# Kernel tuning notes

Hardware: AMD Instinct MI355X
Metric: run time of the kernel (lower is better)

The kernel has to match this reference:

```python
import jax, jax.numpy as jnp
import numpy as np

# ---- dimensions ----
N = 16384      # nodes
E = 131072     # edges (avg degree 8)
F = 128        # scalar channel width == s_dim
L = 9          # spherical-harmonic components (lmax=2)
R = 8          # radial basis size
DOUT = L * F   # post-product node width (1152)
K = 1024       # fixed number of master nodes (static stand-in for m>0.5)
HID = 64       # master-selection hidden dim
DA = 64        # virtual-attention head dim
LAMBDA_ATTN = 0.5
R_CUT = 5.0
EPS = 1e-9


def sh_l2(u):
    # real SH polynomials up to l=2 on unit vectors u[..., 3] -> [..., 9]
    x, y, z = u[..., 0], u[..., 1], u[..., 2]
    o = jnp.ones_like(x)
    return jnp.stack([o, x, y, z, x * y, y * z, 3.0 * z * z - 1.0, x * z, x * x - y * y], axis=-1)


def bessel(r):
    # Bessel radial basis; r [..., 1] -> [..., R]
    n = jnp.arange(1, R + 1, dtype=r.dtype)
    return jnp.sqrt(2.0 / R_CUT) * jnp.sin(n * jnp.pi * r / R_CUT) / jnp.maximum(r, EPS)


def setup_inputs() -> dict:
    key = jax.random.key(0)
    ks = jax.random.split(key, 18)
    s = lambda d: 1.0 / np.sqrt(d)
    return {
        'h': jax.random.normal(ks[0], (N, F), jnp.float32),
        'pos': 3.0 * jax.random.normal(ks[1], (N, 3), jnp.float32),
        'edge_sh': jax.random.normal(ks[2], (E, L), jnp.float32),
        'edge_feats': jax.random.uniform(ks[3], (E, R), jnp.float32),
        'W_node_l': s(F) * jax.random.normal(ks[4], (F, F), jnp.float32),
        'W_rad_l': s(R) * jax.random.normal(ks[5], (R, F), jnp.float32),
        'W_prod_l': s(L * F) * jax.random.normal(ks[6], (L, F, DOUT), jnp.float32),
        'ms_W1': s(F) * jax.random.normal(ks[7], (F, HID), jnp.float32),
        'ms_b1': jnp.zeros((HID,), jnp.float32),
        'ms_W2': s(HID) * jax.random.normal(ks[8], (HID, 1), jnp.float32),
        'ms_b2': jnp.zeros((1,), jnp.float32),
        'vg_Wq': s(F) * jax.random.normal(ks[9], (F, DA), jnp.float32),
        'vg_Wk': s(F) * jax.random.normal(ks[10], (F, DA), jnp.float32),
        'W_node_h': s(DOUT) * jax.random.normal(ks[11], (DOUT, F), jnp.float32),
        'W_rad_h': s(R) * jax.random.normal(ks[12], (R, F), jnp.float32),
        'W_prod_h': s(L * F) * jax.random.normal(ks[13], (L, F, DOUT), jnp.float32),
        'edge_index': jax.random.randint(ks[14], (2, E), 0, N),
    }


def reference(h, pos, edge_sh, edge_feats, W_node_l, W_rad_l, W_prod_l,
              ms_W1, ms_b1, ms_W2, ms_b2, vg_Wq, vg_Wk,
              W_node_h, W_rad_h, W_prod_h, edge_index):
    src, dst = edge_index[0], edge_index[1]

    # ---- local conv + reshape + prod (with padded residual sc) ----
    t = (h[src] @ W_node_l) * (edge_feats @ W_rad_l)                      # [E,F]
    msg = edge_sh[:, :, None] * t[:, None, :]                             # [E,L,F]
    upd = jax.ops.segment_sum(msg, dst, num_segments=N)                   # [N,L,F]
    sc = jnp.pad(h, ((0, 0), (0, DOUT - F)))
    h_local = jnp.einsum('nlf,lfg->ng', upd, W_prod_l) + sc               # [N,DOUT]

    # ---- master selection (MLP -> sigmoid); fixed top-K masters ----
    hs = h_local[:, :F]
    m = jax.nn.sigmoid(jax.nn.relu(hs @ ms_W1 + ms_b1) @ ms_W2 + ms_b2)[:, 0]  # [N]
    _, midx = jax.lax.top_k(m, K)
    master_idx = jnp.sort(midx)                                           # [K]

    # ---- induced subgraph among masters as dense [K,K] adjacency ----
    rank = jnp.full((N,), K, dtype=jnp.int32).at[master_idx].set(jnp.arange(K, dtype=jnp.int32))
    adj = jnp.zeros((K + 1, K + 1), h.dtype).at[rank[src], rank[dst]].max(jnp.ones((E,), h.dtype))
    adj_induced = adj[:K, :K]

    h_m = h_local[master_idx]                                             # [K,DOUT]
    pos_m = pos[master_idx]                                               # [K,3]
    hms = h_m[:, :F]

    # ---- virtual graph generation (attention -> thresholded dense adj) ----
    q = hms @ vg_Wq
    kk = hms @ vg_Wk
    A = jax.nn.sigmoid(q @ kk.T / jnp.sqrt(jnp.asarray(DA, h.dtype)))     # [K,K]
    A_virtual = jnp.where(A > LAMBDA_ATTN, A, 0.0)
    eye = jnp.eye(K, dtype=bool)
    Bv = (A_virtual > 0) & ~eye                                           # remove self loops
    Bv = Bv | Bv.T                                                        # to_undirected
    adj_master = jnp.clip(adj_induced + Bv.astype(h.dtype), 0.0, 1.0) * (1.0 - jnp.eye(K, dtype=h.dtype))

    # ---- hierarchical conv over dense master graph ----
    A_rec = adj_master.T                                                  # A_rec[i,j]=1: sender j -> receiver i
    V = pos_m[None, :, :] - pos_m[:, None, :]                             # vec = pos[src]-pos[dst]
    r = jnp.linalg.norm(V, axis=-1, keepdims=True)                        # [K,K,1]
    u = V / jnp.maximum(r, EPS)
    sh_m = sh_l2(u)                                                       # [K,K,L]
    rad = bessel(r)                                                       # [K,K,R]
    tm = (h_m @ W_node_h)[None, :, :] * (rad @ W_rad_h) * A_rec[:, :, None]  # [K,K,F]
    upd_m = jnp.einsum('ijl,ijf->ilf', sh_m, tm)                          # [K,L,F]
    h_hier = jnp.einsum('ilf,lfg->ig', upd_m, W_prod_h) + h_m             # sc_master pad is 0-width

    # ---- masked scatter blend ----
    h_exp = jnp.zeros_like(h_local).at[master_idx].set(h_hier)
    h_final = (1.0 - m[:, None]) * h_local + m[:, None] * h_exp
    return (h_final, A_virtual, m, master_idx)
```

## Files before the change

### kernel.cpp

```cpp
#include <hip/hip_runtime.h>
#include <hip/hip_bf16.h>
#include <stdint.h>

#define N_NODES 16384
#define E_EDGES 131072
#define F_DIM 128
#define L_DIM 9
#define R_DIM 8
#define DOUT_DIM 1152
#define K_SEL 1024
#define HID_DIM 64
#define DA_DIM 64

typedef unsigned short u16;
typedef __attribute__((ext_vector_type(8))) short bf16x8;
typedef __attribute__((ext_vector_type(4))) float f32x4;

static __device__ inline u16 f2bs(float x) {
  union { __hip_bfloat16 b; u16 s; } u;
  u.b = __float2bfloat16(x);
  return u.s;
}

#define GLDS16(gsrc, ldst) __builtin_amdgcn_global_load_lds( \
    (__attribute__((address_space(1))) void*)(void*)(gsrc),  \
    (__attribute__((address_space(3))) void*)(ldst), 16, 0, 0)

__global__ __launch_bounds__(256) void gemm_mfma(
    const float* __restrict__ A, const u16* __restrict__ Bt,
    float* __restrict__ C, int ldc, int M, int Nc, int Kc,
    const float* __restrict__ Add, int ldadd, int addW)
{
  __shared__ float Af[128 * 32];
  __shared__ u16  Bs[128 * 32];
  const int tid = threadIdx.x;
  const int wave = tid >> 6, lane = tid & 63;
  const int wm = wave >> 1, wn = wave & 1;
  const int l15 = lane & 15, quad = lane >> 4;
  const int bm = blockIdx.y * 128, bn = blockIdx.x * 128;

  f32x4 acc[4][4];
#pragma unroll
  for (int i = 0; i < 4; i++)
#pragma unroll
    for (int j = 0; j < 4; j++) acc[i][j] = (f32x4)(0.f);

  for (int k0 = 0; k0 < Kc; k0 += 32) {
    __syncthreads();
#pragma unroll
    for (int it = 0; it < 4; it++) {
      int c = it * 256 + tid;
      int row = c >> 3, op = c & 7;
      int oct = op ^ (row & 7);
      const float* g = A + (size_t)(bm + row) * Kc + k0 + oct * 4;
      GLDS16(g, &Af[c * 4]);
    }
#pragma unroll
    for (int it = 0; it < 2; it++) {
      int c = it * 256 + tid;
      int row = c >> 2, qp = c & 3;
      int q = qp ^ ((row >> 1) & 3);
      const u16* g = Bt + (size_t)(bn + row) * Kc + k0 + q * 8;
      GLDS16(g, &Bs[c * 8]);
    }
    __syncthreads();

    bf16x8 af[4], bfg[4];
#pragma unroll
    for (int mi = 0; mi < 4; mi++) {
      int m = wm * 64 + mi * 16 + l15;
      int o0 = (quad * 2) ^ (m & 7), o1 = (quad * 2 + 1) ^ (m & 7);
      float4 lo = *(const float4*)&Af[m * 32 + o0 * 4];
      float4 hi = *(const float4*)&Af[m * 32 + o1 * 4];
      bf16x8 r;
      r[0] = (short)f2bs(lo.x); r[1] = (short)f2bs(lo.y);
      r[2] = (short)f2bs(lo.z); r[3] = (short)f2bs(lo.w);
      r[4] = (short)f2bs(hi.x); r[5] = (short)f2bs(hi.y);
      r[6] = (short)f2bs(hi.z); r[7] = (short)f2bs(hi.w);
      af[mi] = r;
    }
#pragma unroll
    for (int ni = 0; ni < 4; ni++) {
      int n = wn * 64 + ni * 16 + l15;
      int q2 = quad ^ ((n >> 1) & 3);
      bfg[ni] = *(const bf16x8*)&Bs[n * 32 + q2 * 8];
    }
#pragma unroll
    for (int mi = 0; mi < 4; mi++)
#pragma unroll
      for (int ni = 0; ni < 4; ni++)
        acc[mi][ni] = __builtin_amdgcn_mfma_f32_16x16x32_bf16(af[mi], bfg[ni], acc[mi][ni], 0, 0, 0);
  }
#pragma unroll
  for (int mi = 0; mi < 4; mi++)
#pragma unroll
    for (int ni = 0; ni < 4; ni++)
#pragma unroll
      for (int r = 0; r < 4; r++) {
        int row = bm + wm * 64 + mi * 16 + quad * 4 + r;
        int col = bn + wn * 64 + ni * 16 + l15;
        float v = acc[mi][ni][r];
        if (Add != nullptr && col < addW) v += Add[(size_t)row * ldadd + col];
        C[(size_t)row * ldc + col] = v;
      }
}

__global__ __launch_bounds__(256) void gemm_mfma_b16(
    const u16* __restrict__ A, const u16* __restrict__ Bt,
    float* __restrict__ C, int ldc, int Kc, int nbx, int nwg,
    const float* __restrict__ Add, int ldadd, int addW)
{
  __shared__ u16 As[2][128 * 32];
  __shared__ u16 Bs[2][128 * 32];
  const int tid = threadIdx.x;
  const int wave = tid >> 6, lane = tid & 63;
  const int wm = wave >> 1, wn = wave & 1;
  const int l15 = lane & 15, quad = lane >> 4;
  const int lin = blockIdx.x;
  const int swz = (lin & 7) * (nwg >> 3) + (lin >> 3);
  const int bm = (swz / nbx) * 128, bn = (swz % nbx) * 128;

  const int c0 = tid,      r0 = c0 >> 2, q0 = (c0 & 3) ^ ((r0 >> 1) & 3);
  const int c1 = 256 + tid, r1 = c1 >> 2, q1 = (c1 & 3) ^ ((r1 >> 1) & 3);
  const u16* gA0 = A + (size_t)(bm + r0) * Kc + q0 * 8;
  const u16* gA1 = A + (size_t)(bm + r1) * Kc + q1 * 8;
  const u16* gB0 = Bt + (size_t)(bn + r0) * Kc + q0 * 8;
  const u16* gB1 = Bt + (size_t)(bn + r1) * Kc + q1 * 8;

  f32x4 acc[4][4];
#pragma unroll
  for (int i = 0; i < 4; i++)
#pragma unroll
    for (int j = 0; j < 4; j++) acc[i][j] = (f32x4)(0.f);

#define STAGE_AB(s, k0) do {                      \
    GLDS16(gA0 + (k0), &As[s][c0 * 8]);           \
    GLDS16(gA1 + (k0), &As[s][c1 * 8]);           \
    GLDS16(gB0 + (k0), &Bs[s][c0 * 8]);           \
    GLDS16(gB1 + (k0), &Bs[s][c1 * 8]);           \
  } while (0)

  STAGE_AB(0, 0);
  __syncthreads();
  int cur = 0;
  const int nt = Kc / 32;
  for (int t = 0; t < nt; t++) {
    if (t + 1 < nt) STAGE_AB(cur ^ 1, (t + 1) * 32);
    bf16x8 af[4], bfg[4];
#pragma unroll
    for (int mi = 0; mi < 4; mi++) {
      int m = wm * 64 + mi * 16 + l15;
      af[mi] = *(const bf16x8*)&As[cur][m * 32 + (quad ^ ((m >> 1) & 3)) * 8];
    }
#pragma unroll
    for (int ni = 0; ni < 4; ni++) {
      int n = wn * 64 + ni * 16 + l15;
      bfg[ni] = *(const bf16x8*)&Bs[cur][n * 32 + (quad ^ ((n >> 1) & 3)) * 8];
    }
#pragma unroll
    for (int mi = 0; mi < 4; mi++)
#pragma unroll
      for (int ni = 0; ni < 4; ni++)
        acc[mi][ni] = __builtin_amdgcn_mfma_f32_16x16x32_bf16(af[mi], bfg[ni], acc[mi][ni], 0, 0, 0);
    __syncthreads();
    cur ^= 1;
  }
#undef STAGE_AB

#pragma unroll
  for (int mi = 0; mi < 4; mi++)
#pragma unroll
    for (int ni = 0; ni < 4; ni++)
#pragma unroll
      for (int r = 0; r < 4; r++) {
        int row = bm + wm * 64 + mi * 16 + quad * 4 + r;
        int col = bn + wn * 64 + ni * 16 + l15;
        float v = acc[mi][ni][r];
        if (Add != nullptr && col < addW) v += Add[(size_t)row * ldadd + col];
        C[(size_t)row * ldc + col] = v;
      }
}

__global__ __launch_bounds__(256) void transpose_bf16(
    const float* __restrict__ W, u16* __restrict__ Bt, int K, int N)
{
  __shared__ float t[32][33];
  const int n0 = blockIdx.x * 32, k0 = blockIdx.y * 32;
  const int tx = threadIdx.x & 31, ty = threadIdx.x >> 5;
  for (int r = ty; r < 32; r += 8) t[r][tx] = W[(size_t)(k0 + r) * N + n0 + tx];
  __syncthreads();
  for (int r = ty; r < 32; r += 8) Bt[(size_t)(n0 + r) * K + k0 + tx] = f2bs(t[tx][r]);
}

__global__ __launch_bounds__(256) void hs_gemm_kernel(
    const float* __restrict__ A,
    const float* __restrict__ B,
    float* __restrict__ psum)
{
  __shared__ float As[16][129];
  __shared__ float Bs[16][128];
  const int tid = threadIdx.x;
  const int tx = tid & 15, ty = tid >> 4;
  const int bm = blockIdx.x * 128;
  const int z = blockIdx.y;
  const int kb = z * (DOUT_DIM / 4);
  const int ke = kb + DOUT_DIM / 4;
  const int ac = tid & 15, ar0 = tid >> 4;
  const int bc = tid & 127, br0 = tid >> 7;
  float acc[8][8];
#pragma unroll
  for (int i = 0; i < 8; i++)
#pragma unroll
    for (int j = 0; j < 8; j++) acc[i][j] = 0.f;

  float ra[8], rb[8];
#define LOADREG(k0) do {                                                       \
    _Pragma("unroll")                                                          \
    for (int rr = 0; rr < 8; rr++)                                             \
      ra[rr] = A[(size_t)(bm + ar0 + rr * 16) * DOUT_DIM + (k0) + ac];         \
    _Pragma("unroll")                                                          \
    for (int rr = 0; rr < 8; rr++)                                             \
      rb[rr] = B[(size_t)((k0) + br0 + rr * 2) * DOUT_DIM + bc];               \
  } while (0)

  LOADREG(kb);
  for (int k0 = kb; k0 < ke; k0 += 16) {
#pragma unroll
    for (int rr = 0; rr < 8; rr++) As[ac][ar0 + rr * 16] = ra[rr];
#pragma unroll
    for (int rr = 0; rr < 8; rr++) Bs[br0 + rr * 2][bc] = rb[rr];
    __syncthreads();
    if (k0 + 16 < ke) LOADREG(k0 + 16);
#pragma unroll
    for (int kk = 0; kk < 16; kk++) {
      float a[8], b[8];
#pragma unroll
      for (int i = 0; i < 8; i++) a[i] = As[kk][ty * 8 + i];
#pragma unroll
      for (int j = 0; j < 8; j++) b[j] = Bs[kk][tx * 8 + j];
#pragma unroll
      for (int i = 0; i < 8; i++)
#pragma unroll
        for (int j = 0; j < 8; j++) acc[i][j] = fmaf(a[i], b[j], acc[i][j]);
    }
    __syncthreads();
  }
#undef LOADREG
#pragma unroll
  for (int i = 0; i < 8; i++) {
    size_t row = (size_t)z * N_NODES + bm + ty * 8 + i;
#pragma unroll
    for (int j = 0; j < 8; j++)
      psum[row * F_DIM + tx * 8 + j] = acc[i][j];
  }
}

__global__ __launch_bounds__(256) void hs_reduce_kernel(
    const float* __restrict__ psum, const float* __restrict__ h, float* __restrict__ hs)
{
  size_t i4 = (size_t)blockIdx.x * 256 + threadIdx.x;
  const size_t stride = (size_t)N_NODES * F_DIM / 4;
  const float4* p = (const float4*)psum;
  float4 a = p[i4], b = p[i4 + stride], c = p[i4 + 2 * stride], d = p[i4 + 3 * stride];
  float4 hh = ((const float4*)h)[i4];
  float4 o;
  o.x = a.x + b.x + c.x + d.x + hh.x;
  o.y = a.y + b.y + c.y + d.y + hh.y;
  o.z = a.z + b.z + c.z + d.z + hh.z;
  o.w = a.w + b.w + c.w + d.w + hh.w;
  ((float4*)hs)[i4] = o;
}

__global__ __launch_bounds__(256) void gemm64_f32(
    const float* __restrict__ A, int lda,
    const float* __restrict__ B, int ldb,
    float* __restrict__ C, int ldc,
    int M, int Nc, int Kc, int kPerSplit,
    const float* __restrict__ Add, int ldadd, int addW)
{
  __shared__ float As[16][65];
  __shared__ float Bs[16][64];
  const int tid = threadIdx.x;
  const int tx = tid & 15, ty = tid >> 4;
  const int bm = blockIdx.y * 64, bn = blockIdx.x * 64;
  const int kb = blockIdx.z * kPerSplit;
  const int ke = min(kb + kPerSplit, Kc);
  float acc[4][4];
#pragma unroll
  for (int i = 0; i < 4; i++)
#pragma unroll
    for (int j = 0; j < 4; j++) acc[i][j] = 0.f;
  for (int k0 = kb; k0 < ke; k0 += 16) {
    const int ac = tid & 15, ar = tid >> 4;
#pragma unroll
    for (int rr = 0; rr < 4; rr++) {
      int row = ar + rr * 16;
      As[ac][row] = A[(size_t)(bm + row) * lda + k0 + ac];
    }
    const int bc = tid & 63, br = tid >> 6;
#pragma unroll
    for (int rr = 0; rr < 4; rr++) {
      int kr = br + rr * 4;
      Bs[kr][bc] = B[(size_t)(k0 + kr) * ldb + bn + bc];
    }
    __syncthreads();
#pragma unroll
    for (int kk = 0; kk < 16; kk++) {
      float a[4], b[4];
#pragma unroll
      for (int i = 0; i < 4; i++) a[i] = As[kk][ty * 4 + i];
#pragma unroll
      for (int j = 0; j < 4; j++) b[j] = Bs[kk][tx * 4 + j];
#pragma unroll
      for (int i = 0; i < 4; i++)
#pragma unroll
        for (int j = 0; j < 4; j++) acc[i][j] = fmaf(a[i], b[j], acc[i][j]);
    }
    __syncthreads();
  }
#pragma unroll
  for (int i = 0; i < 4; i++) {
    int row = bm + ty * 4 + i;
#pragma unroll
    for (int j = 0; j < 4; j++) {
      int col = bn + tx * 4 + j;
      if (gridDim.z > 1) {
        atomicAdd(&C[(size_t)row * ldc + col], acc[i][j]);
      } else {
        float v = acc[i][j];
        if (Add != nullptr && col < addW) v += Add[(size_t)row * ldadd + col];
        C[(size_t)row * ldc + col] = v;
      }
    }
  }
}

__global__ __launch_bounds__(256) void count_kernel(
    const int* __restrict__ ei, int* __restrict__ counts)
{
  int e = blockIdx.x * 256 + threadIdx.x;
  atomicAdd(&counts[ei[E_EDGES + e]], 1);
}

__global__ __launch_bounds__(1024) void scan_kernel(
    const int* __restrict__ counts, int* __restrict__ offsets, int* __restrict__ cursor)
{
  __shared__ int part[1024];
  const int t = threadIdx.x;
  const int base = t * 16;
  int loc[16];
  int s = 0;
#pragma unroll
  for (int k = 0; k < 16; k++) { loc[k] = counts[base + k]; s += loc[k]; }
  part[t] = s;
  __syncthreads();
  for (int d = 1; d < 1024; d <<= 1) {
    int v = (t >= d) ? part[t - d] : 0;
    __syncthreads();
    part[t] += v;
    __syncthreads();
  }
  int run = part[t] - s;
#pragma unroll
  for (int k = 0; k < 16; k++) {
    offsets[base + k] = run;
    cursor[base + k] = run;
    run += loc[k];
  }
}

__global__ __launch_bounds__(256) void fill_kernel(
    const int* __restrict__ ei, int* __restrict__ cursor, int* __restrict__ elist)
{
  int e = blockIdx.x * 256 + threadIdx.x;
  int d = ei[E_EDGES + e];
  int p = atomicAdd(&cursor[d], 1);
  elist[p] = e;
}

__global__ __launch_bounds__(128) void gather_accum_kernel(
    const float* __restrict__ hW, const float* __restrict__ edge_sh,
    const float* __restrict__ edge_feats, const float* __restrict__ W_rad_l,
    const int* __restrict__ ei, const int* __restrict__ offsets,
    const int* __restrict__ counts, const int* __restrict__ elist,
    float* __restrict__ upd, u16* __restrict__ updb)
{
  const int d = blockIdx.x, f = threadIdx.x;
  const float w0 = W_rad_l[0 * F_DIM + f], w1 = W_rad_l[1 * F_DIM + f];
  const float w2 = W_rad_l[2 * F_DIM + f], w3 = W_rad_l[3 * F_DIM + f];
  const float w4 = W_rad_l[4 * F_DIM + f], w5 = W_rad_l[5 * F_DIM + f];
  const float w6 = W_rad_l[6 * F_DIM + f], w7 = W_rad_l[7 * F_DIM + f];
  const int b = offsets[d], n = counts[d];
  float acc[L_DIM];
#pragma unroll
  for (int l = 0; l < L_DIM; l++) acc[l] = 0.f;
  for (int k = 0; k < n; k++) {
    const int e = elist[b + k];
    const int s = ei[e];
    const float4 ef0 = *(const float4*)&edge_feats[(size_t)e * R_DIM];
    const float4 ef1 = *(const float4*)&edge_feats[(size_t)e * R_DIM + 4];
    float rw = ef0.x * w0;
    rw = fmaf(ef0.y, w1, rw); rw = fmaf(ef0.z, w2, rw); rw = fmaf(ef0.w, w3, rw);
    rw = fmaf(ef1.x, w4, rw); rw = fmaf(ef1.y, w5, rw);
    rw = fmaf(ef1.z, w6, rw); rw = fmaf(ef1.w, w7, rw);
    const float tf = hW[(size_t)s * F_DIM + f] * rw;
#pragma unroll
    for (int l = 0; l < L_DIM; l++)
      acc[l] = fmaf(edge_sh[(size_t)e * L_DIM + l], tf, acc[l]);
  }
#pragma unroll
  for (int l = 0; l < L_DIM; l++)
    upd[(size_t)d * DOUT_DIM + l * F_DIM + f] = acc[l];
  if (updb != nullptr) {
#pragma unroll
    for (int l = 0; l < L_DIM; l++)
      updb[(size_t)d * DOUT_DIM + l * F_DIM + f] = f2bs(acc[l]);
  }
}

__global__ __launch_bounds__(256) void gate_kernel(
    const float* __restrict__ hs, const float* __restrict__ W1,
    const float* __restrict__ b1, const float* __restrict__ W2,
    const float* __restrict__ b2, float* __restrict__ m_ws, float* __restrict__ m_out,
    int* __restrict__ hist1)
{
  __shared__ float sW1[F_DIM * HID_DIM];
  __shared__ float srow[4][F_DIM];
  const int tid = threadIdx.x;
  for (int t = tid; t < F_DIM * HID_DIM; t += 256) sW1[t] = W1[t];
  const int wave = tid >> 6, lane = tid & 63;
  const int n = blockIdx.x * 4 + wave;
  srow[wave][lane] = hs[(size_t)n * F_DIM + lane];
  srow[wave][lane + 64] = hs[(size_t)n * F_DIM + lane + 64];
  __syncthreads();
  float hid = b1[lane];
#pragma unroll 8
  for (int c = 0; c < F_DIM; c++) hid = fmaf(srow[wave][c], sW1[c * HID_DIM + lane], hid);
  hid = fmaxf(hid, 0.f);
  float v = hid * W2[lane];
#pragma unroll
  for (int off = 32; off > 0; off >>= 1) v += __shfl_down(v, off);
  if (lane == 0) {
    float mm = 1.f / (1.f + expf(-(v + b2[0])));
    m_ws[n] = mm;
    m_out[n] = mm;
    unsigned mb = __float_as_uint(mm);
    atomicAdd(&hist1[mb >> 16], 1);
  }
}

__global__ __launch_bounds__(1024) void radix_sel_kernel(
    const int* __restrict__ hist, const int* __restrict__ kin, int kinIdx,
    int* __restrict__ outp, int outIdx)
{
  __shared__ int part[1024];
  const int t = threadIdx.x;
  const int Kv = kin ? kin[kinIdx] : K_SEL;
  const int base = t * 64;
  int s = 0;
  for (int k = 0; k < 64; k++) s += hist[base + k];
  part[t] = s;
  __syncthreads();
  for (int d = 1; d < 1024; d <<= 1) {
    int v = (t + d < 1024) ? part[t + d] : 0;
    __syncthreads();
    part[t] += v;
    __syncthreads();
  }
  int inc = part[t];
  if (inc >= Kv && inc - s < Kv) {
    int r = inc - s;
    for (int b = base + 63; b >= base; b--) {
      int hv = hist[b];
      if (r + hv >= Kv) { outp[outIdx] = b; outp[outIdx + 1] = Kv - r; break; }
      r += hv;
    }
  }
}

__global__ __launch_bounds__(256) void hist2_kernel(
    const float* __restrict__ m_ws, const int* __restrict__ selb, int* __restrict__ hist2)
{
  int i = blockIdx.x * 256 + threadIdx.x;
  unsigned mb = __float_as_uint(m_ws[i]);
  if ((int)(mb >> 16) == selb[0]) atomicAdd(&hist2[mb & 0xFFFFu], 1);
}

__global__ __launch_bounds__(256) void flag_kernel(
    const float* __restrict__ m_ws, int* __restrict__ selb,
    unsigned char* __restrict__ flags, int* __restrict__ cand)
{
  int i = blockIdx.x * 256 + threadIdx.x;
  unsigned mb = __float_as_uint(m_ws[i]);
  unsigned vb = ((unsigned)selb[0] << 16) | (unsigned)selb[2];
  unsigned char fl = 0;
  if (mb > vb) fl = 1;
  else if (mb == vb) { int p = atomicAdd(&selb[4], 1); cand[p] = i; }
  flags[i] = fl;
}

__global__ __launch_bounds__(1024) void cand_kernel(
    const int* __restrict__ selb, const int* __restrict__ cand, unsigned char* __restrict__ flags)
{
  const int nc = selb[4], need = selb[3];
  for (int c = threadIdx.x; c < nc; c += 1024) {
    const int idx = cand[c];
    int r = 0;
    for (int o = 0; o < nc; o++) r += (cand[o] < idx) ? 1 : 0;
    if (r < need) flags[idx] = 1;
  }
}

__global__ __launch_bounds__(1024) void compact_kernel(
    const unsigned char* __restrict__ flags, int* __restrict__ midx,
    int* __restrict__ rank, float* __restrict__ mi_out)
{
  __shared__ int part[1024];
  const int t = threadIdx.x;
  const int base = t * 16;
  int loc[16];
  int s = 0;
#pragma unroll
  for (int k = 0; k < 16; k++) { loc[k] = flags[base + k]; s += loc[k]; }
  part[t] = s;
  __syncthreads();
  for (int d = 1; d < 1024; d <<= 1) {
    int v = (t >= d) ? part[t - d] : 0;
    __syncthreads();
    part[t] += v;
    __syncthreads();
  }
  int run = part[t] - s;
#pragma unroll
  for (int k = 0; k < 16; k++) {
    int i = base + k;
    if (loc[k]) {
      midx[run] = i;
      mi_out[run] = (float)i;
      rank[i] = run;
      run++;
    } else {
      rank[i] = K_SEL;
    }
  }
}

__global__ __launch_bounds__(256) void adj_kernel(
    const int* __restrict__ ei, const int* __restrict__ rank,
    unsigned char* __restrict__ adjm, unsigned char* __restrict__ adjT)
{
  int e = blockIdx.x * 256 + threadIdx.x;
  int rs = rank[ei[e]];
  int rd = rank[ei[E_EDGES + e]];
  if (rs < K_SEL && rd < K_SEL) {
    adjm[(size_t)rs * K_SEL + rd] = 1;
    adjT[(size_t)rd * K_SEL + rs] = 1;
  }
}

__global__ __launch_bounds__(128) void gather_kernel(
    const float* __restrict__ hl, const float* __restrict__ pos,
    const int* __restrict__ midx, float* __restrict__ h_m, float* __restrict__ pos_m)
{
  const int rI = blockIdx.x, t = threadIdx.x;
  const int mi = midx[rI];
  const float4* src = (const float4*)(hl + (size_t)mi * DOUT_DIM);
  float4* dst = (float4*)(h_m + (size_t)rI * DOUT_DIM);
  for (int c = t; c < DOUT_DIM / 4; c += 128) dst[c] = src[c];
  if (t < 3) pos_m[rI * 3 + t] = pos[mi * 3 + t];
}

__global__ __launch_bounds__(128) void qk_kernel(
    const float* __restrict__ hs, const int* __restrict__ midx,
    const float* __restrict__ Wq, const float* __restrict__ Wk,
    float* __restrict__ q, float* __restrict__ kk)
{
  __shared__ float row[F_DIM];
  const int i = blockIdx.x, t = threadIdx.x;
  const int mi = midx[i];
  row[t] = hs[(size_t)mi * F_DIM + t];
  __syncthreads();
  const int d = t & 63;
  const float* W = (t < 64) ? Wq : Wk;
  float acc = 0.f;
#pragma unroll 8
  for (int c = 0; c < F_DIM; c++) acc = fmaf(row[c], W[c * DA_DIM + d], acc);
  float* dst = (t < 64) ? q : kk;
  dst[(size_t)i * DA_DIM + d] = acc;
}

__global__ __launch_bounds__(256) void attn_kernel(
    const float* __restrict__ q, const float* __restrict__ kk,
    unsigned char* __restrict__ maskA, unsigned char* __restrict__ maskAT,
    float* __restrict__ Av)
{
  __shared__ float qs[16][DA_DIM + 1], ks[16][DA_DIM + 1];
  const int tx = threadIdx.x, ty = threadIdx.y;
  const int tid = ty * 16 + tx;
  const int i0 = blockIdx.y * 16, j0 = blockIdx.x * 16;
  for (int t = tid; t < 16 * DA_DIM; t += 256) {
    int rr = t >> 6, cc = t & 63;
    qs[rr][cc] = q[(size_t)(i0 + rr) * DA_DIM + cc];
    ks[rr][cc] = kk[(size_t)(j0 + rr) * DA_DIM + cc];
  }
  __syncthreads();
  float acc = 0.f;
#pragma unroll
  for (int d2 = 0; d2 < DA_DIM; d2++) acc = fmaf(qs[ty][d2], ks[tx][d2], acc);
  float sgl = 1.f / (1.f + expf(-acc * 0.125f));
  size_t o = (size_t)(i0 + ty) * K_SEL + (j0 + tx);
  bool big = sgl > 0.5f;
  unsigned char bb = big ? 1 : 0;
  maskA[o] = bb;
  maskAT[(size_t)(j0 + tx) * K_SEL + (i0 + ty)] = bb;
  Av[o] = big ? sgl : 0.f;
}

__global__ __launch_bounds__(256) void listbuild_kernel(
    const unsigned char* __restrict__ adjT, const unsigned char* __restrict__ maskAT,
    const unsigned char* __restrict__ maskA, u16* __restrict__ list, int* __restrict__ nj)
{
  __shared__ int cnt;
  const int i = blockIdx.x, tid = threadIdx.x;
  const int lane = tid & 63;
  if (tid == 0) cnt = 0;
  __syncthreads();
  const int j0 = tid * 4;
  uchar4 a  = *(const uchar4*)&adjT  [(size_t)i * K_SEL + j0];
  uchar4 mt = *(const uchar4*)&maskAT[(size_t)i * K_SEL + j0];
  uchar4 ma = *(const uchar4*)&maskA [(size_t)i * K_SEL + j0];
  unsigned char av[4];
  av[0] = a.x | mt.x | ma.x; av[1] = a.y | mt.y | ma.y;
  av[2] = a.z | mt.z | ma.z; av[3] = a.w | mt.w | ma.w;
#pragma unroll
  for (int r = 0; r < 4; r++) {
    int j = j0 + r;
    bool e = (j != i) && av[r];
    unsigned long long m = __ballot(e);
    int nset = __popcll(m);
    int base = 0;
    if (lane == 0 && nset) base = atomicAdd(&cnt, nset);
    base = __shfl(base, 0);
    if (e) {
      int p = base + __popcll(m & ((1ull << lane) - 1ull));
      list[(size_t)i * K_SEL + p] = (u16)j;
    }
  }
  __syncthreads();
  if (tid == 0) nj[i] = cnt;
}

__global__ __launch_bounds__(256) void hier2_kernel(
    const float* __restrict__ hWn, const float* __restrict__ pos_m,
    const float* __restrict__ W_rad_h, const u16* __restrict__ list,
    const int* __restrict__ nj, float* __restrict__ psum2)
{
  __shared__ float gsm[128][20];
  __shared__ float red[L_DIM][F_DIM];
  const int tid = threadIdx.x;
  const int i = blockIdx.x >> 1, half = blockIdx.x & 1;
  const int f = tid & 127, jsub = tid >> 7;
  const float sw0 = W_rad_h[0 * F_DIM + f], sw1 = W_rad_h[1 * F_DIM + f];
  const float sw2 = W_rad_h[2 * F_DIM + f], sw3 = W_rad_h[3 * F_DIM + f];
  const float sw4 = W_rad_h[4 * F_DIM + f], sw5 = W_rad_h[5 * F_DIM + f];
  const float sw6 = W_rad_h[6 * F_DIM + f], sw7 = W_rad_h[7 * F_DIM + f];
  const float* hWf = hWn + f;
  const float pix = pos_m[i * 3 + 0], piy = pos_m[i * 3 + 1], piz = pos_m[i * 3 + 2];
  float acc[L_DIM];
#pragma unroll
  for (int l = 0; l < L_DIM; l++) acc[l] = 0.f;
  const int n = nj[i];

#define HBODY(tt)                                                        \
  { float2 s2 = *(const float2*)&gsm[tt][16];                            \
    const int jj = __float_as_int(s2.y);                                 \
    const float hw = hWf[(size_t)jj * F_DIM];                            \
    float4 r0 = *(const float4*)&gsm[tt][0];                             \
    float4 r1 = *(const float4*)&gsm[tt][4];                             \
    float4 s0 = *(const float4*)&gsm[tt][8];                             \
    float4 s1g = *(const float4*)&gsm[tt][12];                           \
    float rw = r0.x * sw0;                                               \
    rw = fmaf(r0.y, sw1, rw); rw = fmaf(r0.z, sw2, rw);                  \
    rw = fmaf(r0.w, sw3, rw); rw = fmaf(r1.x, sw4, rw);                  \
    rw = fmaf(r1.y, sw5, rw); rw = fmaf(r1.z, sw6, rw);                  \
    rw = fmaf(r1.w, sw7, rw);                                            \
    const float tm = hw * rw;                                            \
    acc[0] = fmaf(s0.x, tm, acc[0]); acc[1] = fmaf(s0.y, tm, acc[1]);    \
    acc[2] = fmaf(s0.z, tm, acc[2]); acc[3] = fmaf(s0.w, tm, acc[3]);    \
    acc[4] = fmaf(s1g.x, tm, acc[4]); acc[5] = fmaf(s1g.y, tm, acc[5]);  \
    acc[6] = fmaf(s1g.z, tm, acc[6]); acc[7] = fmaf(s1g.w, tm, acc[7]);  \
    acc[8] = fmaf(s2.x, tm, acc[8]); }

  for (int c0 = half * 128; c0 < n; c0 += 256) {
    const int cnt = min(128, n - c0);
    __syncthreads();
    if (tid < cnt) {
      const int j = list[(size_t)i * K_SEL + c0 + tid];
      float vx = pos_m[j * 3 + 0] - pix;
      float vy = pos_m[j * 3 + 1] - piy;
      float vz = pos_m[j * 3 + 2] - piz;
      float r = sqrtf(vx * vx + vy * vy + vz * vz);
      float rm = fmaxf(r, 1e-9f);
      float inv = 1.f / rm;
      float ux = vx * inv, uy = vy * inv, uz = vz * inv;
      float theta = 0.62831853071795864769f * r;
      float s1 = sinf(theta), c1 = cosf(theta);
      float coef = 0.632455532033675866f * inv;
      float snm2 = 0.f, snm1 = s1;
      gsm[tid][0] = s1 * coef;
#pragma unroll
      for (int nn = 2; nn <= R_DIM; nn++) {
        float sn = 2.f * c1 * snm1 - snm2;
        gsm[tid][nn - 1] = sn * coef;
        snm2 = snm1; snm1 = sn;
      }
      gsm[tid][8] = 1.f; gsm[tid][9] = ux; gsm[tid][10] = uy; gsm[tid][11] = uz;
      gsm[tid][12] = ux * uy; gsm[tid][13] = uy * uz;
      gsm[tid][14] = 3.f * uz * uz - 1.f;
      gsm[tid][15] = ux * uz; gsm[tid][16] = ux * ux - uy * uy;
      gsm[tid][17] = __int_as_float(j);
    }
    __syncthreads();
    int t = jsub;
    for (; t + 2 < cnt; t += 4) { HBODY(t); HBODY(t + 2); }
    for (; t < cnt; t += 2) { HBODY(t); }
  }
#undef HBODY
  __syncthreads();
  if (jsub == 1) {
#pragma unroll
    for (int l = 0; l < L_DIM; l++) red[l][f] = acc[l];
  }
  __syncthreads();
  if (jsub == 0) {
#pragma unroll
    for (int l = 0; l < L_DIM; l++)
      psum2[((size_t)half * K_SEL + i) * DOUT_DIM + l * F_DIM + f] = acc[l] + red[l][f];
  }
}

__global__ __launch_bounds__(256) void hier_fin_kernel(
    const float* __restrict__ psum2, u16* __restrict__ updbm)
{
  size_t idx = (size_t)blockIdx.x * 256 + threadIdx.x;
  updbm[idx] = f2bs(psum2[idx] + psum2[idx + (size_t)K_SEL * DOUT_DIM]);
}

__global__ __launch_bounds__(256) void combine_kernel(
    float* __restrict__ out0, const float* __restrict__ h_hier,
    const float* __restrict__ m_ws, const int* __restrict__ rank)
{
  size_t i4 = (size_t)blockIdx.x * 256 + threadIdx.x;
  int n = (int)(i4 / (DOUT_DIM / 4));
  int g4 = (int)(i4 % (DOUT_DIM / 4));
  float mv = m_ws[n];
  int r = rank[n];
  float4 hl = ((const float4*)out0)[i4];
  float4 he = make_float4(0.f, 0.f, 0.f, 0.f);
  if (r < K_SEL) he = ((const float4*)h_hier)[(size_t)r * (DOUT_DIM / 4) + g4];
  float4 o;
  o.x = (1.f - mv) * hl.x + mv * he.x;
  o.y = (1.f - mv) * hl.y + mv * he.y;
  o.z = (1.f - mv) * hl.z + mv * he.z;
  o.w = (1.f - mv) * hl.w + mv * he.w;
  ((float4*)out0)[i4] = o;
}

extern "C" void kernel_launch(void* const* d_in, const int* in_sizes, int n_in,
                              void* d_out, int out_size, void* d_ws, size_t ws_size,
                              hipStream_t stream)
{
  const float* h         = (const float*)d_in[0];
  const float* pos       = (const float*)d_in[1];
  const float* edge_sh   = (const float*)d_in[2];
  const float* edge_feats= (const float*)d_in[3];
  const float* W_node_l  = (const float*)d_in[4];
  const float* W_rad_l   = (const float*)d_in[5];
  const float* W_prod_l  = (const float*)d_in[6];
  const float* ms_W1     = (const float*)d_in[7];
  const float* ms_b1     = (const float*)d_in[8];
  const float* ms_W2     = (const float*)d_in[9];
  const float* ms_b2     = (const float*)d_in[10];
  const float* vg_Wq     = (const float*)d_in[11];
  const float* vg_Wk     = (const float*)d_in[12];
  const float* W_node_h  = (const float*)d_in[13];
  const float* W_rad_h   = (const float*)d_in[14];
  const float* W_prod_h  = (const float*)d_in[15];
  const int*   eidx      = (const int*)d_in[16];

  float* out    = (float*)d_out;
  float* out_hf = out;
  float* out_Av = out + (size_t)N_NODES * DOUT_DIM;
  float* out_m  = out_Av + (size_t)K_SEL * K_SEL;
  float* out_mi = out_m + N_NODES;

  char* ws = (char*)d_ws;
  float* upd = (float*)ws;
  float* hW  = (float*)(ws + (size_t)N_NODES * DOUT_DIM * 4);
  float* hs  = hW;
  const size_t updbOff = (size_t)N_NODES * DOUT_DIM * 4 + (size_t)N_NODES * F_DIM * 4;
  const size_t updbNeed = updbOff + (size_t)N_NODES * DOUT_DIM * 2;
  const bool useB16 = (ws_size >= updbNeed);
  u16* updb = (u16*)(ws + updbOff);
  float* psum = out_hf;
  u16* Btl = (u16*)out_Av;
  char* csr = (char*)out_Av + (((size_t)DOUT_DIM * DOUT_DIM * 2 + 255) & ~(size_t)255);
  int* counts  = (int*)csr;
  int* offsets = counts + N_NODES;
  int* cursor  = offsets + N_NODES;
  int* elist   = cursor + N_NODES;
  size_t off = 0;
  auto alloc = [&](size_t bytes) -> void* {
    void* p = ws + off;
    off += (bytes + 255) & ~(size_t)255;
    return p;
  };
  float* m_ws  = (float*)alloc((size_t)N_NODES * 4);
  int*   rank  = (int*)alloc((size_t)N_NODES * 4);
  int*   midx  = (int*)alloc((size_t)K_SEL * 4);
  int*   hist1 = (int*)alloc((size_t)65536 * 4);
  int*   hist2 = (int*)alloc((size_t)65536 * 4);
  int*   selb  = (int*)alloc((size_t)64 * 4);
  int*   cand  = (int*)alloc((size_t)N_NODES * 4);
  unsigned char* flags = (unsigned char*)alloc((size_t)N_NODES);
  unsigned char* adjm  = (unsigned char*)alloc((size_t)K_SEL * K_SEL);
  unsigned char* adjT  = (unsigned char*)alloc((size_t)K_SEL * K_SEL);
  unsigned char* maskA = (unsigned char*)alloc((size_t)K_SEL * K_SEL);
  unsigned char* maskAT= (unsigned char*)alloc((size_t)K_SEL * K_SEL);
  float* qbuf  = (float*)alloc((size_t)K_SEL * DA_DIM * 4);
  float* kbuf  = (float*)alloc((size_t)K_SEL * DA_DIM * 4);
  float* h_m   = (float*)alloc((size_t)K_SEL * DOUT_DIM * 4);
  float* pos_m = (float*)alloc((size_t)K_SEL * 3 * 4);
  float* hWn   = (float*)alloc((size_t)K_SEL * F_DIM * 4);
  float* psum2 = (float*)alloc((size_t)2 * K_SEL * DOUT_DIM * 4);
  float* h_hier= (float*)alloc((size_t)K_SEL * DOUT_DIM * 4);
  u16*   Bth   = (u16*)alloc((size_t)DOUT_DIM * DOUT_DIM * 2);
  u16*   jlist = (u16*)alloc((size_t)K_SEL * K_SEL * 2);
  int*   njbuf = (int*)alloc((size_t)K_SEL * 4);
  u16*   updbm = (u16*)alloc((size_t)K_SEL * DOUT_DIM * 2);

  hipMemsetAsync(counts, 0, (size_t)N_NODES * 4, stream);
  transpose_bf16<<<dim3(DOUT_DIM / 32, DOUT_DIM / 32), 256, 0, stream>>>(
      W_prod_l, Btl, DOUT_DIM, DOUT_DIM);
  gemm64_f32<<<dim3(F_DIM / 64, N_NODES / 64, 1), 256, 0, stream>>>(
      h, F_DIM, W_node_l, F_DIM, hW, F_DIM, N_NODES, F_DIM, F_DIM, F_DIM, nullptr, 0, 0);
  count_kernel<<<E_EDGES / 256, 256, 0, stream>>>(eidx, counts);
  scan_kernel<<<1, 1024, 0, stream>>>(counts, offsets, cursor);
  fill_kernel<<<E_EDGES / 256, 256, 0, stream>>>(eidx, cursor, elist);
  gather_accum_kernel<<<N_NODES, 128, 0, stream>>>(
      hW, edge_sh, edge_feats, W_rad_l, eidx, offsets, counts, elist, upd,
      useB16 ? updb : nullptr);
  hs_gemm_kernel<<<dim3(N_NODES / 128, 4), 256, 0, stream>>>(upd, W_prod_l, psum);
  hs_reduce_kernel<<<(N_NODES * F_DIM / 4) / 256, 256, 0, stream>>>(psum, h, hs);
  if (useB16) {
    gemm_mfma_b16<<<(DOUT_DIM / 128) * (N_NODES / 128), 256, 0, stream>>>(
        updb, Btl, out_hf, DOUT_DIM, DOUT_DIM, DOUT_DIM / 128,
        (DOUT_DIM / 128) * (N_NODES / 128), h, F_DIM, F_DIM);
  } else {
    gemm_mfma<<<dim3(DOUT_DIM / 128, N_NODES / 128), 256, 0, stream>>>(
        upd, Btl, out_hf, DOUT_DIM, N_NODES, DOUT_DIM, DOUT_DIM, h, F_DIM, F_DIM);
  }

  hipMemsetAsync(adjm, 0, (size_t)2 * K_SEL * K_SEL, stream);
  hipMemsetAsync(hist1, 0, (size_t)65536 * 4 * 2 + 256, stream);
  transpose_bf16<<<dim3(DOUT_DIM / 32, DOUT_DIM / 32), 256, 0, stream>>>(
      W_prod_h, Bth, DOUT_DIM, DOUT_DIM);
  gate_kernel<<<N_NODES / 4, 256, 0, stream>>>(hs, ms_W1, ms_b1, ms_W2, ms_b2,
                                               m_ws, out_m, hist1);
  radix_sel_kernel<<<1, 1024, 0, stream>>>(hist1, nullptr, 0, selb, 0);
  hist2_kernel<<<N_NODES / 256, 256, 0, stream>>>(m_ws, selb, hist2);
  radix_sel_kernel<<<1, 1024, 0, stream>>>(hist2, selb, 1, selb, 2);
  flag_kernel<<<N_NODES / 256, 256, 0, stream>>>(m_ws, selb, flags, cand);
  cand_kernel<<<1, 1024, 0, stream>>>(selb, cand, flags);
  compact_kernel<<<1, 1024, 0, stream>>>(flags, midx, rank, out_mi);
  adj_kernel<<<E_EDGES / 256, 256, 0, stream>>>(eidx, rank, adjm, adjT);
  gather_kernel<<<K_SEL, 128, 0, stream>>>(out_hf, pos, midx, h_m, pos_m);
  qk_kernel<<<K_SEL, 128, 0, stream>>>(hs, midx, vg_Wq, vg_Wk, qbuf, kbuf);
  attn_kernel<<<dim3(K_SEL / 16, K_SEL / 16), dim3(16, 16), 0, stream>>>(
      qbuf, kbuf, maskA, maskAT, out_Av);
  listbuild_kernel<<<K_SEL, 256, 0, stream>>>(adjT, maskAT, maskA, jlist, njbuf);
  hipMemsetAsync(hWn, 0, (size_t)K_SEL * F_DIM * 4, stream);
  gemm64_f32<<<dim3(F_DIM / 64, K_SEL / 64, 4), 256, 0, stream>>>(
      h_m, DOUT_DIM, W_node_h, F_DIM, hWn, F_DIM,
      K_SEL, F_DIM, DOUT_DIM, DOUT_DIM / 4, nullptr, 0, 0);
  hier2_kernel<<<K_SEL * 2, 256, 0, stream>>>(hWn, pos_m, W_rad_h, jlist, njbuf, psum2);
  hier_fin_kernel<<<(K_SEL * DOUT_DIM) / 256, 256, 0, stream>>>(psum2, updbm);
  gemm_mfma_b16<<<(DOUT_DIM / 128) * (K_SEL / 128), 256, 0, stream>>>(
      updbm, Bth, h_hier, DOUT_DIM, DOUT_DIM, DOUT_DIM / 128,
      (DOUT_DIM / 128) * (K_SEL / 128), h_m, DOUT_DIM, DOUT_DIM);
  combine_kernel<<<(N_NODES * DOUT_DIM / 4) / 256, 256, 0, stream>>>(out_hf, h_hier, m_ws, rank);
}
```

Baseline: 678.1 us.

## Split master-graph neighbor loop into per-chunk blocks with atomic accumulation

```diff
diff --git a/kernel.cpp b/kernel.cpp
--- a/kernel.cpp
+++ b/kernel.cpp
@@ -650,26 +650,57 @@
   if (tid == 0) nj[i] = cnt;
 }
 
-__global__ __launch_bounds__(256) void hier2_kernel(
+__global__ __launch_bounds__(128) void hier3_kernel(
     const float* __restrict__ hWn, const float* __restrict__ pos_m,
     const float* __restrict__ W_rad_h, const u16* __restrict__ list,
-    const int* __restrict__ nj, float* __restrict__ psum2)
+    const int* __restrict__ nj, float* __restrict__ upd_m)
 {
   __shared__ float gsm[128][20];
-  __shared__ float red[L_DIM][F_DIM];
-  const int tid = threadIdx.x;
-  const int i = blockIdx.x >> 1, half = blockIdx.x & 1;
-  const int f = tid & 127, jsub = tid >> 7;
+  const int bid = blockIdx.x;
+  const int i = bid >> 3, ch = bid & 7;
+  const int n = nj[i];
+  const int c0 = ch * 128;
+  if (c0 >= n) return;
+  const int cnt = min(128, n - c0);
+  const int f = threadIdx.x;
   const float sw0 = W_rad_h[0 * F_DIM + f], sw1 = W_rad_h[1 * F_DIM + f];
   const float sw2 = W_rad_h[2 * F_DIM + f], sw3 = W_rad_h[3 * F_DIM + f];
   const float sw4 = W_rad_h[4 * F_DIM + f], sw5 = W_rad_h[5 * F_DIM + f];
   const float sw6 = W_rad_h[6 * F_DIM + f], sw7 = W_rad_h[7 * F_DIM + f];
   const float* hWf = hWn + f;
   const float pix = pos_m[i * 3 + 0], piy = pos_m[i * 3 + 1], piz = pos_m[i * 3 + 2];
+
+  if (f < cnt) {
+    const int j = list[(size_t)i * K_SEL + c0 + f];
+    float vx = pos_m[j * 3 + 0] - pix;
+    float vy = pos_m[j * 3 + 1] - piy;
+    float vz = pos_m[j * 3 + 2] - piz;
+    float r = sqrtf(vx * vx + vy * vy + vz * vz);
+    float rm = fmaxf(r, 1e-9f);
+    float inv = 1.f / rm;
+    float ux = vx * inv, uy = vy * inv, uz = vz * inv;
+    float theta = 0.62831853071795864769f * r;
+    float s1 = sinf(theta), c1 = cosf(theta);
+    float coef = 0.632455532033675866f * inv;
+    float snm2 = 0.f, snm1 = s1;
+    gsm[f][0] = s1 * coef;
+#pragma unroll
+    for (int nn = 2; nn <= R_DIM; nn++) {
+      float sn = 2.f * c1 * snm1 - snm2;
+      gsm[f][nn - 1] = sn * coef;
+      snm2 = snm1; snm1 = sn;
+    }
+    gsm[f][8] = 1.f; gsm[f][9] = ux; gsm[f][10] = uy; gsm[f][11] = uz;
+    gsm[f][12] = ux * uy; gsm[f][13] = uy * uz;
+    gsm[f][14] = 3.f * uz * uz - 1.f;
+    gsm[f][15] = ux * uz; gsm[f][16] = ux * ux - uy * uy;
+    gsm[f][17] = __int_as_float(j);
+  }
+  __syncthreads();
+
   float acc[L_DIM];
 #pragma unroll
   for (int l = 0; l < L_DIM; l++) acc[l] = 0.f;
-  const int n = nj[i];
 
 #define HBODY(tt)                                                        \
   { float2 s2 = *(const float2*)&gsm[tt][16];                            \
@@ -691,59 +722,21 @@
     acc[6] = fmaf(s1g.z, tm, acc[6]); acc[7] = fmaf(s1g.w, tm, acc[7]);  \
     acc[8] = fmaf(s2.x, tm, acc[8]); }
 
-  for (int c0 = half * 128; c0 < n; c0 += 256) {
-    const int cnt = min(128, n - c0);
-    __syncthreads();
-    if (tid < cnt) {
-      const int j = list[(size_t)i * K_SEL + c0 + tid];
-      float vx = pos_m[j * 3 + 0] - pix;
-      float vy = pos_m[j * 3 + 1] - piy;
-      float vz = pos_m[j * 3 + 2] - piz;
-      float r = sqrtf(vx * vx + vy * vy + vz * vz);
-      float rm = fmaxf(r, 1e-9f);
-      float inv = 1.f / rm;
-      float ux = vx * inv, uy = vy * inv, uz = vz * inv;
-      float theta = 0.62831853071795864769f * r;
-      float s1 = sinf(theta), c1 = cosf(theta);
-      float coef = 0.632455532033675866f * inv;
-      float snm2 = 0.f, snm1 = s1;
-      gsm[tid][0] = s1 * coef;
-#pragma unroll
-      for (int nn = 2; nn <= R_DIM; nn++) {
-        float sn = 2.f * c1 * snm1 - snm2;
-        gsm[tid][nn - 1] = sn * coef;
-        snm2 = snm1; snm1 = sn;
-      }
-      gsm[tid][8] = 1.f; gsm[tid][9] = ux; gsm[tid][10] = uy; gsm[tid][11] = uz;
-      gsm[tid][12] = ux * uy; gsm[tid][13] = uy * uz;
-      gsm[tid][14] = 3.f * uz * uz - 1.f;
-      gsm[tid][15] = ux * uz; gsm[tid][16] = ux * ux - uy * uy;
-      gsm[tid][17] = __int_as_float(j);
-    }
-    __syncthreads();
-    int t = jsub;
-    for (; t + 2 < cnt; t += 4) { HBODY(t); HBODY(t + 2); }
-    for (; t < cnt; t += 2) { HBODY(t); }
-  }
+  int t = 0;
+  for (; t + 1 < cnt; t += 2) { HBODY(t); HBODY(t + 1); }
+  for (; t < cnt; t++) { HBODY(t); }
 #undef HBODY
-  __syncthreads();
-  if (jsub == 1) {
-#pragma unroll
-    for (int l = 0; l < L_DIM; l++) red[l][f] = acc[l];
-  }
-  __syncthreads();
-  if (jsub == 0) {
-#pragma unroll
-    for (int l = 0; l < L_DIM; l++)
-      psum2[((size_t)half * K_SEL + i) * DOUT_DIM + l * F_DIM + f] = acc[l] + red[l][f];
-  }
-}
-
-__global__ __launch_bounds__(256) void hier_fin_kernel(
-    const float* __restrict__ psum2, u16* __restrict__ updbm)
+
+#pragma unroll
+  for (int l = 0; l < L_DIM; l++)
+    atomicAdd(&upd_m[(size_t)i * DOUT_DIM + l * F_DIM + f], acc[l]);
+}
+
+__global__ __launch_bounds__(256) void cast_bf16_kernel(
+    const float* __restrict__ x, u16* __restrict__ y)
 {
   size_t idx = (size_t)blockIdx.x * 256 + threadIdx.x;
-  updbm[idx] = f2bs(psum2[idx] + psum2[idx + (size_t)K_SEL * DOUT_DIM]);
+  y[idx] = f2bs(x[idx]);
 }
 
 __global__ __launch_bounds__(256) void combine_kernel(
@@ -832,7 +825,7 @@
   float* h_m   = (float*)alloc((size_t)K_SEL * DOUT_DIM * 4);
   float* pos_m = (float*)alloc((size_t)K_SEL * 3 * 4);
   float* hWn   = (float*)alloc((size_t)K_SEL * F_DIM * 4);
-  float* psum2 = (float*)alloc((size_t)2 * K_SEL * DOUT_DIM * 4);
+  float* upd_m = (float*)alloc((size_t)K_SEL * DOUT_DIM * 4);
   float* h_hier= (float*)alloc((size_t)K_SEL * DOUT_DIM * 4);
   u16*   Bth   = (u16*)alloc((size_t)DOUT_DIM * DOUT_DIM * 2);
   u16*   jlist = (u16*)alloc((size_t)K_SEL * K_SEL * 2);
@@ -863,6 +856,7 @@
 
   hipMemsetAsync(adjm, 0, (size_t)2 * K_SEL * K_SEL, stream);
   hipMemsetAsync(hist1, 0, (size_t)65536 * 4 * 2 + 256, stream);
+  hipMemsetAsync(upd_m, 0, (size_t)K_SEL * DOUT_DIM * 4, stream);
   transpose_bf16<<<dim3(DOUT_DIM / 32, DOUT_DIM / 32), 256, 0, stream>>>(
       W_prod_h, Bth, DOUT_DIM, DOUT_DIM);
   gate_kernel<<<N_NODES / 4, 256, 0, stream>>>(hs, ms_W1, ms_b1, ms_W2, ms_b2,
@@ -883,8 +877,8 @@
   gemm64_f32<<<dim3(F_DIM / 64, K_SEL / 64, 4), 256, 0, stream>>>(
       h_m, DOUT_DIM, W_node_h, F_DIM, hWn, F_DIM,
       K_SEL, F_DIM, DOUT_DIM, DOUT_DIM / 4, nullptr, 0, 0);
-  hier2_kernel<<<K_SEL * 2, 256, 0, stream>>>(hWn, pos_m, W_rad_h, jlist, njbuf, psum2);
-  hier_fin_kernel<<<(K_SEL * DOUT_DIM) / 256, 256, 0, stream>>>(psum2, updbm);
+  hier3_kernel<<<K_SEL * 8, 128, 0, stream>>>(hWn, pos_m, W_rad_h, jlist, njbuf, upd_m);
+  cast_bf16_kernel<<<(K_SEL * DOUT_DIM) / 256, 256, 0, stream>>>(upd_m, updbm);
   gemm_mfma_b16<<<(DOUT_DIM / 128) * (K_SEL / 128), 256, 0, stream>>>(
       updbm, Bth, h_hier, DOUT_DIM, DOUT_DIM, DOUT_DIM / 128,
       (DOUT_DIM / 128) * (K_SEL / 128), h_m, DOUT_DIM, DOUT_DIM);
```

After: 676.7 us. No clear change (-0.2%).
